# Performance work log

Hardware: AMD Instinct MI355X
Metric: run time of the kernel (lower is better)

## Reference

```python
import jax, jax.numpy as jnp
import numpy as np

B, T, C = 8, 2048, 768
N_LAYER, LAYER_ID = 12, 0


def setup_inputs() -> dict:
    key = jax.random.key(0)
    ks = jax.random.split(key, 5)
    s = 1.0 / np.sqrt(C)
    x = jax.random.normal(ks[0], (B, T, C), jnp.float32)
    Wk = jax.random.normal(ks[1], (C, C), jnp.float32) * s
    Wv = jax.random.normal(ks[2], (C, C), jnp.float32) * s
    Wr = jax.random.normal(ks[3], (C, C), jnp.float32) * s
    Wo = jax.random.normal(ks[4], (C, C), jnp.float32) * s
    # 'fancy' init for decay / first (layer_id=0 -> ratio_0_to_1 = 0)
    h = np.arange(C, dtype=np.float64)
    decay = (-5.0 + 8.0 * (h / (C - 1)) ** 0.7).astype(np.float32)
    zigzag = (((np.arange(C) + 1) % 3) - 1).astype(np.float64) * 0.5
    first = (np.log(0.3) + zigzag).astype(np.float32)
    return dict(x=x, Wk=Wk, Wv=Wv, Wr=Wr, Wo=Wo,
                decay=jnp.asarray(decay), first=jnp.asarray(first))


def _bi_wkv(w, u, k, v):
    """Bidirectional WKV (Vision-RWKV style), numerically stabilized scans.

    y_t = (sum_{i<t} e^{-(t-1-i)w + k_i} v_i + sum_{i>t} e^{-(i-1-t)w + k_i} v_i
           + e^{u + k_t} v_t) / (same with v_i -> 1).
    k, v: [B,T,C]; w, u: [C].
    """
    kT = jnp.swapaxes(k, 0, 1)  # [T,B,C]
    vT = jnp.swapaxes(v, 0, 1)
    Bb, Cc = kT.shape[1], kT.shape[2]
    NEG = jnp.float32(-1e38)

    def step(carry, inp):
        a, b, p = carry  # a = sum e^{x_i-p} v_i, b = sum e^{x_i-p}, p = running max
        kt, vt = inp
        out = (a, b, p)  # state covers strictly-earlier positions
        p_new = jnp.maximum(p - w, kt)
        e1 = jnp.exp(p - w - p_new)
        e2 = jnp.exp(kt - p_new)
        return (e1 * a + e2 * vt, e1 * b + e2, p_new), out

    init = (jnp.zeros((Bb, Cc), jnp.float32),
            jnp.zeros((Bb, Cc), jnp.float32),
            jnp.full((Bb, Cc), NEG, jnp.float32))
    _, (aL, bL, pL) = jax.lax.scan(step, init, (kT, vT))
    _, (aR, bR, pR) = jax.lax.scan(step, init, (kT[::-1], vT[::-1]))
    aR, bR, pR = aR[::-1], bR[::-1], pR[::-1]

    ps = u + kT  # self term exponent
    q = jnp.maximum(jnp.maximum(pL, pR), ps)
    eL = jnp.exp(pL - q)
    eR = jnp.exp(pR - q)
    eS = jnp.exp(ps - q)
    y = (eL * aL + eR * aR + eS * vT) / (eL * bL + eR * bR + eS)
    return jnp.swapaxes(y, 0, 1)  # [B,T,C]


def reference(x, Wk, Wv, Wr, Wo, decay, first):
    Tlen = x.shape[1]
    # shift_pixel=0 -> xk = xv = xr = x
    k = jnp.einsum('btc,oc->bto', x, Wk)
    v = jnp.einsum('btc,oc->bto', x, Wv)
    sr = jax.nn.sigmoid(jnp.einsum('btc,oc->bto', x, Wr))
    y = _bi_wkv(decay / Tlen, first / Tlen, k, v)
    return jnp.einsum('btj,cj->btc', sr * y, Wo)
```

## Files before the change

kernel.cpp:

```cpp
#include <hip/hip_runtime.h>

#define BSZ 8
#define TLEN 2048
#define CDIM 768
#define LCH 16
#define NCH (TLEN / LCH)

typedef __attribute__((ext_vector_type(4))) float f32x4;
typedef __attribute__((ext_vector_type(8))) _Float16 f16x8;
typedef __attribute__((ext_vector_type(4))) _Float16 f16x4;
typedef __attribute__((ext_vector_type(4))) float float4v;

#define GLD16(g, l)                                                          \
    __builtin_amdgcn_global_load_lds(                                        \
        (const __attribute__((address_space(1))) unsigned int*)(g),          \
        (__attribute__((address_space(3))) unsigned int*)(l), 16, 0, 0)

__global__ __launch_bounds__(256) void split_f16(const float* __restrict__ src,
                                                 _Float16* __restrict__ dst, int n4) {
    int i = blockIdx.x * 256 + threadIdx.x;
    if (i >= n4) return;
    float4v f = ((const float4v*)src)[i];
    f16x4 h;
    #pragma unroll
    for (int j = 0; j < 4; ++j) h[j] = (_Float16)f[j];
    ((f16x4*)dst)[i] = h;
}

__global__ __launch_bounds__(256, 2) void gemm_128(
    const _Float16* __restrict__ A, const _Float16* __restrict__ W,
    _Float16* __restrict__ o0, _Float16* __restrict__ o1, _Float16* __restrict__ o2,
    float* __restrict__ of32, int mpx, int NTL) {
    constexpr int K = CDIM;
    constexpr int NT = K / 64;
    __shared__ __align__(16) char smem[65536];

    const int tid  = threadIdx.x;
    const int lane = tid & 63;
    const int wid  = tid >> 6;
    const int bid  = blockIdx.x;
    const int xcd  = bid & 7;
    const int lj   = bid >> 3;
    const int mt   = lj / NTL;
    const int nt   = lj - mt * NTL;
    const int m0   = (xcd * mpx + mt) * 128;
    const int n0   = nt * 128;

    const int gq = (tid & 7) ^ ((tid >> 3) & 7);
    const char* gA = (const char*)A;
    const char* gW = (const char*)W;
    const size_t gofsA = (size_t)(m0 + (tid >> 3)) * (K * 2) + gq * 16;
    const size_t gofsB = (size_t)(n0 + (tid >> 3)) * (K * 2) + gq * 16;
    const int lofs = tid * 16;

    auto STAGE = [&](int bufb, int t) {
        const size_t kb = (size_t)t * 128;
        #pragma unroll
        for (int q = 0; q < 4; ++q) {
            GLD16(gA + gofsA + kb + (size_t)q * 49152, &smem[bufb] + lofs + q * 4096);
            GLD16(gW + gofsB + kb + (size_t)q * 49152, &smem[bufb + 16384] + lofs + q * 4096);
        }
    };

    const int wr = wid >> 1, wc = wid & 1;
    const int rl = lane & 15;
    const int kc0 = ((((lane >> 4)    ) ^ (rl & 7)) << 4);
    const int kc1 = ((((lane >> 4) + 4) ^ (rl & 7)) << 4);

    f32x4 acc[4][4];
    #pragma unroll
    for (int i = 0; i < 4; ++i)
        #pragma unroll
        for (int j = 0; j < 4; ++j)
            acc[i][j] = (f32x4){0.f, 0.f, 0.f, 0.f};

    auto COMPUTE = [&](int bufb) {
        const char* sa = &smem[bufb];
        const char* sbb = &smem[bufb + 16384];
        #pragma unroll
        for (int ks = 0; ks < 2; ++ks) {
            const int kc = ks ? kc1 : kc0;
            f16x8 a[4], b[4];
            #pragma unroll
            for (int fi = 0; fi < 4; ++fi)
                a[fi] = *(const f16x8*)(sa + (wr * 64 + fi * 16 + rl) * 128 + kc);
            #pragma unroll
            for (int fj = 0; fj < 4; ++fj)
                b[fj] = *(const f16x8*)(sbb + (wc * 64 + fj * 16 + rl) * 128 + kc);
            #pragma unroll
            for (int fi = 0; fi < 4; ++fi)
                #pragma unroll
                for (int fj = 0; fj < 4; ++fj)
                    acc[fi][fj] = __builtin_amdgcn_mfma_f32_16x16x32_f16(
                        a[fi], b[fj], acc[fi][fj], 0, 0, 0);
        }
    };

    STAGE(0, 0);
    __syncthreads();
    int buf = 0;
    for (int t = 0; t < NT; ++t) {
        if (t + 1 < NT) STAGE(buf ^ 32768, t + 1);
        COMPUTE(buf);
        __syncthreads();
        buf ^= 32768;
    }

    const int erow0 = m0 + wr * 64 + ((lane >> 4) << 2);
    if (of32) {
        const int col0 = n0 + wc * 64 + rl;
        #pragma unroll
        for (int mf = 0; mf < 4; ++mf)
            #pragma unroll
            for (int nf = 0; nf < 4; ++nf)
                #pragma unroll
                for (int r = 0; r < 4; ++r)
                    of32[(size_t)(erow0 + mf * 16 + r) * CDIM + (col0 + nf * 16)] =
                        acc[mf][nf][r];
    } else {
        const int mat  = nt / 6;
        const int col0 = (nt - mat * 6) * 128 + wc * 64 + rl;
        _Float16* o = (mat == 0) ? o0 : ((mat == 1) ? o1 : o2);
        if (mat == 2) {
            #pragma unroll
            for (int mf = 0; mf < 4; ++mf)
                #pragma unroll
                for (int nf = 0; nf < 4; ++nf)
                    #pragma unroll
                    for (int r = 0; r < 4; ++r)
                        o[(size_t)(erow0 + mf * 16 + r) * CDIM + (col0 + nf * 16)] =
                            (_Float16)(1.0f / (1.0f + __expf(-acc[mf][nf][r])));
        } else {
            #pragma unroll
            for (int mf = 0; mf < 4; ++mf)
                #pragma unroll
                for (int nf = 0; nf < 4; ++nf)
                    #pragma unroll
                    for (int r = 0; r < 4; ++r)
                        o[(size_t)(erow0 + mf * 16 + r) * CDIM + (col0 + nf * 16)] =
                            (_Float16)acc[mf][nf][r];
        }
    }
}

#define WKV_STEP(a, bb, p, kt, vt, w)                \
    {                                                \
        const float pn = fmaxf((p) - (w), (kt));     \
        const float e1 = __expf((p) - (w) - pn);     \
        const float e2 = __expf((kt) - pn);          \
        (a)  = e1 * (a)  + e2 * (vt);                \
        (bb) = e1 * (bb) + e2;                       \
        (p)  = pn;                                   \
    }

__global__ __launch_bounds__(256) void wkv_phase1(
    const _Float16* __restrict__ k, const _Float16* __restrict__ v,
    const float* __restrict__ decay,
    float* __restrict__ Sfa, float* __restrict__ Sfb, float* __restrict__ Sfp,
    float* __restrict__ Sba, float* __restrict__ Sbb, float* __restrict__ Sbp) {
    const int c = blockIdx.x * 256 + threadIdx.x;
    const int j = blockIdx.y;
    const int b = blockIdx.z;
    const float w = decay[c] * (1.0f / (float)TLEN);

    const size_t base = ((size_t)b * TLEN + (size_t)j * LCH) * CDIM + c;
    float kt[LCH], vt[LCH];
    #pragma unroll
    for (int i = 0; i < LCH; ++i) {
        kt[i] = (float)k[base + (size_t)i * CDIM];
        vt[i] = (float)v[base + (size_t)i * CDIM];
    }

    const size_t idx = ((size_t)b * NCH + j) * CDIM + c;

    float a = 0.0f, bb = 0.0f, p = -1e38f;
    #pragma unroll
    for (int i = 0; i < LCH; ++i) WKV_STEP(a, bb, p, kt[i], vt[i], w);
    Sfa[idx] = a; Sfb[idx] = bb; Sfp[idx] = p;

    a = 0.0f; bb = 0.0f; p = -1e38f;
    #pragma unroll
    for (int i = LCH - 1; i >= 0; --i) WKV_STEP(a, bb, p, kt[i], vt[i], w);
    Sba[idx] = a; Sbb[idx] = bb; Sbp[idx] = p;
}

#define WKV_COMBINE(a, bb, p, as, bs, ps, wL)        \
    {                                                \
        const float pn = fmaxf((p) - (wL), (ps));    \
        const float e1 = __expf((p) - (wL) - pn);    \
        const float e2 = __expf((ps) - pn);          \
        (a)  = e1 * (a)  + e2 * (as);                \
        (bb) = e1 * (bb) + e2 * (bs);                \
        (p)  = pn;                                   \
    }

__global__ __launch_bounds__(64) void wkv_phase2(
    const float* __restrict__ Sfa, const float* __restrict__ Sfb, const float* __restrict__ Sfp,
    const float* __restrict__ Sba, const float* __restrict__ Sbb, const float* __restrict__ Sbp,
    const float* __restrict__ decay,
    float* __restrict__ Lina, float* __restrict__ Linb, float* __restrict__ Linp,
    float* __restrict__ Rina, float* __restrict__ Rinb, float* __restrict__ Rinp) {
    const int c = blockIdx.x * 64 + threadIdx.x;
    const int b = blockIdx.y;
    const int dir = blockIdx.z;
    const float wL = decay[c] * ((float)LCH / (float)TLEN);

    const float* Sa = dir ? Sba : Sfa;
    const float* Sb = dir ? Sbb : Sfb;
    const float* Sp = dir ? Sbp : Sfp;
    float* Oa = dir ? Rina : Lina;
    float* Ob = dir ? Rinb : Linb;
    float* Op = dir ? Rinp : Linp;

    const size_t base = (size_t)b * NCH * CDIM + c;
    auto IDX = [&](int j) {
        return base + (size_t)(dir ? (NCH - 1 - j) : j) * CDIM;
    };

    float gaA[4], gbA[4], gpA[4], gaB[4], gbB[4], gpB[4];
    #pragma unroll
    for (int u = 0; u < 4; ++u) {
        const size_t id = IDX(u);
        gaA[u] = Sa[id]; gbA[u] = Sb[id]; gpA[u] = Sp[id];
    }
    float a = 0.0f, bb = 0.0f, p = -1e38f;

    for (int jg = 0; jg < NCH; jg += 8) {
        #pragma unroll
        for (int u = 0; u < 4; ++u) {
            const size_t id = IDX(jg + 4 + u);
            gaB[u] = Sa[id]; gbB[u] = Sb[id]; gpB[u] = Sp[id];
        }
        #pragma unroll
        for (int u = 0; u < 4; ++u) {
            const size_t id = IDX(jg + u);
            Oa[id] = a; Ob[id] = bb; Op[id] = p;
            WKV_COMBINE(a, bb, p, gaA[u], gbA[u], gpA[u], wL);
        }
        if (jg + 8 < NCH) {
            #pragma unroll
            for (int u = 0; u < 4; ++u) {
                const size_t id = IDX(jg + 8 + u);
                gaA[u] = Sa[id]; gbA[u] = Sb[id]; gpA[u] = Sp[id];
            }
        }
        #pragma unroll
        for (int u = 0; u < 4; ++u) {
            const size_t id = IDX(jg + 4 + u);
            Oa[id] = a; Ob[id] = bb; Op[id] = p;
            WKV_COMBINE(a, bb, p, gaB[u], gbB[u], gpB[u], wL);
        }
    }
}

__global__ __launch_bounds__(256) void wkv_phase3(
    const _Float16* __restrict__ k, const _Float16* __restrict__ v,
    const _Float16* __restrict__ sr,
    const float* __restrict__ Lina, const float* __restrict__ Linb, const float* __restrict__ Linp,
    const float* __restrict__ Rina, const float* __restrict__ Rinb, const float* __restrict__ Rinp,
    const float* __restrict__ decay, const float* __restrict__ first,
    _Float16* __restrict__ zh) {
    const int c = blockIdx.x * 256 + threadIdx.x;
    const int j = blockIdx.y;
    const int b = blockIdx.z;
    const float w = decay[c] * (1.0f / (float)TLEN);
    const float u = first[c] * (1.0f / (float)TLEN);

    const size_t base = ((size_t)b * TLEN + (size_t)j * LCH) * CDIM + c;
    float kt[LCH], vt[LCH];
    #pragma unroll
    for (int i = 0; i < LCH; ++i) {
        kt[i] = (float)k[base + (size_t)i * CDIM];
        vt[i] = (float)v[base + (size_t)i * CDIM];
    }

    const size_t idx = ((size_t)b * NCH + j) * CDIM + c;

    float ar[LCH], br[LCH], pr[LCH];
    {
        float a = Rina[idx], bb = Rinb[idx], p = Rinp[idx];
        #pragma unroll
        for (int i = LCH - 1; i >= 0; --i) {
            ar[i] = a; br[i] = bb; pr[i] = p;
            WKV_STEP(a, bb, p, kt[i], vt[i], w);
        }
    }
    {
        float a = Lina[idx], bb = Linb[idx], p = Linp[idx];
        #pragma unroll
        for (int i = 0; i < LCH; ++i) {
            const size_t off = base + (size_t)i * CDIM;
            const float srt = (float)sr[off];
            const float ps = u + kt[i];
            const float q  = fmaxf(fmaxf(p, pr[i]), ps);
            const float eL = __expf(p - q);
            const float eR = __expf(pr[i] - q);
            const float eS = __expf(ps - q);
            const float num = eL * a  + eR * ar[i] + eS * vt[i];
            const float den = eL * bb + eR * br[i] + eS;
            zh[off] = (_Float16)(srt * (num / den));
            WKV_STEP(a, bb, p, kt[i], vt[i], w);
        }
    }
}

extern "C" void kernel_launch(void* const* d_in, const int* in_sizes, int n_in,
                              void* d_out, int out_size, void* d_ws, size_t ws_size,
                              hipStream_t stream) {
    const float* x     = (const float*)d_in[0];
    const float* Wk    = (const float*)d_in[1];
    const float* Wv    = (const float*)d_in[2];
    const float* Wr    = (const float*)d_in[3];
    const float* Wo    = (const float*)d_in[4];
    const float* decay = (const float*)d_in[5];
    const float* first = (const float*)d_in[6];
    float* out = (float*)d_out;

    const size_t WN = (size_t)CDIM * CDIM;
    const size_t wbytes = 4 * WN * sizeof(_Float16);
    const size_t per_b  = (size_t)TLEN * CDIM * 8 + 12ull * NCH * CDIM * 4;
    if (ws_size < wbytes + per_b) return;
    int nb = (int)((ws_size - wbytes) / per_b);
    if (nb > BSZ) nb = BSZ;

    _Float16* wsp  = (_Float16*)d_ws;
    _Float16* Wcat = wsp;
    _Float16* Woh  = wsp + 3 * WN;

    const size_t NE = (size_t)nb * TLEN * CDIM;
    const size_t NP = (size_t)nb * NCH * CDIM;
    float* Sfa = (float*)(wsp + 4 * WN);
    float* Sfb = Sfa + NP;  float* Sfp = Sfb + NP;
    float* Sba = Sfp + NP;  float* Sbb = Sba + NP;  float* Sbp = Sbb + NP;
    float* Lina = Sbp + NP; float* Linb = Lina + NP; float* Linp = Linb + NP;
    float* Rina = Linp + NP; float* Rinb = Rina + NP; float* Rinp = Rinb + NP;
    _Float16* kh  = (_Float16*)(Rinp + NP);
    _Float16* vh  = kh + NE;
    _Float16* srh = vh + NE;
    _Float16* xh  = srh + NE;
    _Float16* zh  = xh;

    split_f16<<<dim3((int)(WN / 1024)), dim3(256), 0, stream>>>(Wk, Wcat + 0 * WN, (int)(WN / 4));
    split_f16<<<dim3((int)(WN / 1024)), dim3(256), 0, stream>>>(Wv, Wcat + 1 * WN, (int)(WN / 4));
    split_f16<<<dim3((int)(WN / 1024)), dim3(256), 0, stream>>>(Wr, Wcat + 2 * WN, (int)(WN / 4));
    split_f16<<<dim3((int)(WN / 1024)), dim3(256), 0, stream>>>(Wo, Woh, (int)(WN / 4));

    for (int b0 = 0; b0 < BSZ; b0 += nb) {
        const int curb = (BSZ - b0 < nb) ? (BSZ - b0) : nb;
        const int rows = curb * TLEN;
        const float* xc = x   + (size_t)b0 * TLEN * CDIM;
        float*       oc = out + (size_t)b0 * TLEN * CDIM;

        const int n4 = rows * CDIM / 4;
        split_f16<<<dim3(n4 / 256), dim3(256), 0, stream>>>(xc, xh, n4);

        const int mtiles = rows / 128;
        const int mpx    = mtiles / 8;

        gemm_128<<<dim3(mtiles * 18), dim3(256), 0, stream>>>(
            xh, Wcat, kh, vh, srh, nullptr, mpx, 18);

        wkv_phase1<<<dim3(CDIM / 256, NCH, curb), dim3(256), 0, stream>>>(
            kh, vh, decay, Sfa, Sfb, Sfp, Sba, Sbb, Sbp);
        wkv_phase2<<<dim3(CDIM / 64, curb, 2), dim3(64), 0, stream>>>(
            Sfa, Sfb, Sfp, Sba, Sbb, Sbp, decay,
            Lina, Linb, Linp, Rina, Rinb, Rinp);
        wkv_phase3<<<dim3(CDIM / 256, NCH, curb), dim3(256), 0, stream>>>(
            kh, vh, srh, Lina, Linb, Linp, Rina, Rinb, Rinp, decay, first, zh);

        gemm_128<<<dim3(mtiles * 6), dim3(256), 0, stream>>>(
            zh, Woh, nullptr, nullptr, nullptr, oc, mpx, 6);
    }
}
```

Measured before the change: 169.6 us.

## Vectorize WKV phases to two channels per thread and merge weight conversions

Measured after the change: 178.8 us. 1.05x slower.

```diff
diff --git a/kernel.cpp b/kernel.cpp
--- a/kernel.cpp
+++ b/kernel.cpp
@@ -10,6 +10,24 @@
 typedef __attribute__((ext_vector_type(8))) _Float16 f16x8;
 typedef __attribute__((ext_vector_type(4))) _Float16 f16x4;
 typedef __attribute__((ext_vector_type(4))) float float4v;
+typedef __attribute__((ext_vector_type(2))) float float2v;
+
+__device__ __forceinline__ float lo16(unsigned u) {
+    unsigned short s = (unsigned short)u;
+    _Float16 h; __builtin_memcpy(&h, &s, 2);
+    return (float)h;
+}
+__device__ __forceinline__ float hi16(unsigned u) {
+    unsigned short s = (unsigned short)(u >> 16);
+    _Float16 h; __builtin_memcpy(&h, &s, 2);
+    return (float)h;
+}
+__device__ __forceinline__ unsigned packf16(float x, float y) {
+    _Float16 hx = (_Float16)x, hy = (_Float16)y;
+    unsigned short sx, sy;
+    __builtin_memcpy(&sx, &hx, 2); __builtin_memcpy(&sy, &hy, 2);
+    return (unsigned)sx | ((unsigned)sy << 16);
+}
 
 #define GLD16(g, l)                                                          \
     __builtin_amdgcn_global_load_lds(                                        \
@@ -20,6 +38,22 @@
                                                  _Float16* __restrict__ dst, int n4) {
     int i = blockIdx.x * 256 + threadIdx.x;
     if (i >= n4) return;
+    float4v f = ((const float4v*)src)[i];
+    f16x4 h;
+    #pragma unroll
+    for (int j = 0; j < 4; ++j) h[j] = (_Float16)f[j];
+    ((f16x4*)dst)[i] = h;
+}
+
+__global__ __launch_bounds__(256) void split_w4(
+    const float* __restrict__ Wk, const float* __restrict__ Wv,
+    const float* __restrict__ Wr, const float* __restrict__ Wo,
+    _Float16* __restrict__ Wcat, _Float16* __restrict__ Woh, int n4) {
+    int i = blockIdx.x * 256 + threadIdx.x;
+    if (i >= n4) return;
+    const int plane = blockIdx.y;
+    const float* src = (plane == 0) ? Wk : (plane == 1) ? Wv : (plane == 2) ? Wr : Wo;
+    _Float16* dst = (plane < 3) ? (Wcat + (size_t)plane * CDIM * CDIM) : Woh;
     float4v f = ((const float4v*)src)[i];
     f16x4 h;
     #pragma unroll
@@ -41,8 +75,8 @@
     const int bid  = blockIdx.x;
     const int xcd  = bid & 7;
     const int lj   = bid >> 3;
-    const int mt   = lj / NTL;
-    const int nt   = lj - mt * NTL;
+    const int nt   = lj / mpx;
+    const int mt   = lj - nt * mpx;
     const int m0   = (xcd * mpx + mt) * 128;
     const int n0   = nt * 128;
 
@@ -153,35 +187,50 @@
         (p)  = pn;                                   \
     }
 
-__global__ __launch_bounds__(256) void wkv_phase1(
+__global__ __launch_bounds__(384) void wkv_phase1(
     const _Float16* __restrict__ k, const _Float16* __restrict__ v,
     const float* __restrict__ decay,
     float* __restrict__ Sfa, float* __restrict__ Sfb, float* __restrict__ Sfp,
     float* __restrict__ Sba, float* __restrict__ Sbb, float* __restrict__ Sbp) {
-    const int c = blockIdx.x * 256 + threadIdx.x;
-    const int j = blockIdx.y;
-    const int b = blockIdx.z;
-    const float w = decay[c] * (1.0f / (float)TLEN);
-
-    const size_t base = ((size_t)b * TLEN + (size_t)j * LCH) * CDIM + c;
-    float kt[LCH], vt[LCH];
+    const int c0 = threadIdx.x * 2;
+    const int j = blockIdx.x;
+    const int b = blockIdx.y;
+    const float2v d2 = *(const float2v*)(decay + c0);
+    const float w0 = d2.x * (1.0f / (float)TLEN);
+    const float w1 = d2.y * (1.0f / (float)TLEN);
+
+    const size_t base = ((size_t)b * TLEN + (size_t)j * LCH) * CDIM + c0;
+    unsigned kt2[LCH], vt2[LCH];
     #pragma unroll
     for (int i = 0; i < LCH; ++i) {
-        kt[i] = (float)k[base + (size_t)i * CDIM];
-        vt[i] = (float)v[base + (size_t)i * CDIM];
-    }
-
-    const size_t idx = ((size_t)b * NCH + j) * CDIM + c;
-
-    float a = 0.0f, bb = 0.0f, p = -1e38f;
-    #pragma unroll
-    for (int i = 0; i < LCH; ++i) WKV_STEP(a, bb, p, kt[i], vt[i], w);
-    Sfa[idx] = a; Sfb[idx] = bb; Sfp[idx] = p;
-
-    a = 0.0f; bb = 0.0f; p = -1e38f;
-    #pragma unroll
-    for (int i = LCH - 1; i >= 0; --i) WKV_STEP(a, bb, p, kt[i], vt[i], w);
-    Sba[idx] = a; Sbb[idx] = bb; Sbp[idx] = p;
+        kt2[i] = *(const unsigned*)(k + base + (size_t)i * CDIM);
+        vt2[i] = *(const unsigned*)(v + base + (size_t)i * CDIM);
+    }
+
+    const size_t idx = ((size_t)b * NCH + j) * CDIM + c0;
+
+    {
+        float a0 = 0.f, b0 = 0.f, p0 = -1e38f, a1 = 0.f, b1 = 0.f, p1 = -1e38f;
+        #pragma unroll
+        for (int i = 0; i < LCH; ++i) {
+            WKV_STEP(a0, b0, p0, lo16(kt2[i]), lo16(vt2[i]), w0);
+            WKV_STEP(a1, b1, p1, hi16(kt2[i]), hi16(vt2[i]), w1);
+        }
+        *(float2v*)(Sfa + idx) = (float2v){a0, a1};
+        *(float2v*)(Sfb + idx) = (float2v){b0, b1};
+        *(float2v*)(Sfp + idx) = (float2v){p0, p1};
+    }
+    {
+        float a0 = 0.f, b0 = 0.f, p0 = -1e38f, a1 = 0.f, b1 = 0.f, p1 = -1e38f;
+        #pragma unroll
+        for (int i = LCH - 1; i >= 0; --i) {
+            WKV_STEP(a0, b0, p0, lo16(kt2[i]), lo16(vt2[i]), w0);
+            WKV_STEP(a1, b1, p1, hi16(kt2[i]), hi16(vt2[i]), w1);
+        }
+        *(float2v*)(Sba + idx) = (float2v){a0, a1};
+        *(float2v*)(Sbb + idx) = (float2v){b0, b1};
+        *(float2v*)(Sbp + idx) = (float2v){p0, p1};
+    }
 }
 
 #define WKV_COMBINE(a, bb, p, as, bs, ps, wL)        \
@@ -200,10 +249,12 @@
     const float* __restrict__ decay,
     float* __restrict__ Lina, float* __restrict__ Linb, float* __restrict__ Linp,
     float* __restrict__ Rina, float* __restrict__ Rinb, float* __restrict__ Rinp) {
-    const int c = blockIdx.x * 64 + threadIdx.x;
+    const int c0 = (blockIdx.x * 64 + threadIdx.x) * 2;
     const int b = blockIdx.y;
     const int dir = blockIdx.z;
-    const float wL = decay[c] * ((float)LCH / (float)TLEN);
+    const float2v d2 = *(const float2v*)(decay + c0);
+    const float wL0 = d2.x * ((float)LCH / (float)TLEN);
+    const float wL1 = d2.y * ((float)LCH / (float)TLEN);
 
     const float* Sa = dir ? Sba : Sfa;
     const float* Sb = dir ? Sbb : Sfb;
@@ -212,94 +263,136 @@
     float* Ob = dir ? Rinb : Linb;
     float* Op = dir ? Rinp : Linp;
 
-    const size_t base = (size_t)b * NCH * CDIM + c;
+    const size_t base = (size_t)b * NCH * CDIM + c0;
     auto IDX = [&](int j) {
         return base + (size_t)(dir ? (NCH - 1 - j) : j) * CDIM;
     };
 
-    float gaA[4], gbA[4], gpA[4], gaB[4], gbB[4], gpB[4];
+    float2v gaA[4], gbA[4], gpA[4], gaB[4], gbB[4], gpB[4];
     #pragma unroll
     for (int u = 0; u < 4; ++u) {
         const size_t id = IDX(u);
-        gaA[u] = Sa[id]; gbA[u] = Sb[id]; gpA[u] = Sp[id];
-    }
-    float a = 0.0f, bb = 0.0f, p = -1e38f;
+        gaA[u] = *(const float2v*)(Sa + id);
+        gbA[u] = *(const float2v*)(Sb + id);
+        gpA[u] = *(const float2v*)(Sp + id);
+    }
+    float a0 = 0.f, b0 = 0.f, p0 = -1e38f, a1 = 0.f, b1 = 0.f, p1 = -1e38f;
 
     for (int jg = 0; jg < NCH; jg += 8) {
         #pragma unroll
         for (int u = 0; u < 4; ++u) {
             const size_t id = IDX(jg + 4 + u);
-            gaB[u] = Sa[id]; gbB[u] = Sb[id]; gpB[u] = Sp[id];
+            gaB[u] = *(const float2v*)(Sa + id);
+            gbB[u] = *(const float2v*)(Sb + id);
+            gpB[u] = *(const float2v*)(Sp + id);
         }
         #pragma unroll
         for (int u = 0; u < 4; ++u) {
             const size_t id = IDX(jg + u);
-            Oa[id] = a; Ob[id] = bb; Op[id] = p;
-            WKV_COMBINE(a, bb, p, gaA[u], gbA[u], gpA[u], wL);
+            *(float2v*)(Oa + id) = (float2v){a0, a1};
+            *(float2v*)(Ob + id) = (float2v){b0, b1};
+            *(float2v*)(Op + id) = (float2v){p0, p1};
+            WKV_COMBINE(a0, b0, p0, gaA[u].x, gbA[u].x, gpA[u].x, wL0);
+            WKV_COMBINE(a1, b1, p1, gaA[u].y, gbA[u].y, gpA[u].y, wL1);
         }
         if (jg + 8 < NCH) {
             #pragma unroll
             for (int u = 0; u < 4; ++u) {
                 const size_t id = IDX(jg + 8 + u);
-                gaA[u] = Sa[id]; gbA[u] = Sb[id]; gpA[u] = Sp[id];
+                gaA[u] = *(const float2v*)(Sa + id);
+                gbA[u] = *(const float2v*)(Sb + id);
+                gpA[u] = *(const float2v*)(Sp + id);
             }
         }
         #pragma unroll
         for (int u = 0; u < 4; ++u) {
             const size_t id = IDX(jg + 4 + u);
-            Oa[id] = a; Ob[id] = bb; Op[id] = p;
-            WKV_COMBINE(a, bb, p, gaB[u], gbB[u], gpB[u], wL);
-        }
-    }
-}
-
-__global__ __launch_bounds__(256) void wkv_phase3(
+            *(float2v*)(Oa + id) = (float2v){a0, a1};
+            *(float2v*)(Ob + id) = (float2v){b0, b1};
+            *(float2v*)(Op + id) = (float2v){p0, p1};
+            WKV_COMBINE(a0, b0, p0, gaB[u].x, gbB[u].x, gpB[u].x, wL0);
+            WKV_COMBINE(a1, b1, p1, gaB[u].y, gbB[u].y, gpB[u].y, wL1);
+        }
+    }
+}
+
+__global__ __launch_bounds__(384) void wkv_phase3(
     const _Float16* __restrict__ k, const _Float16* __restrict__ v,
     const _Float16* __restrict__ sr,
     const float* __restrict__ Lina, const float* __restrict__ Linb, const float* __restrict__ Linp,
     const float* __restrict__ Rina, const float* __restrict__ Rinb, const float* __restrict__ Rinp,
     const float* __restrict__ decay, const float* __restrict__ first,
     _Float16* __restrict__ zh) {
-    const int c = blockIdx.x * 256 + threadIdx.x;
-    const int j = blockIdx.y;
-    const int b = blockIdx.z;
-    const float w = decay[c] * (1.0f / (float)TLEN);
-    const float u = first[c] * (1.0f / (float)TLEN);
-
-    const size_t base = ((size_t)b * TLEN + (size_t)j * LCH) * CDIM + c;
-    float kt[LCH], vt[LCH];
+    const int c0 = threadIdx.x * 2;
+    const int j = blockIdx.x;
+    const int b = blockIdx.y;
+    const float2v d2 = *(const float2v*)(decay + c0);
+    const float2v f2 = *(const float2v*)(first + c0);
+    const float w0 = d2.x * (1.0f / (float)TLEN);
+    const float w1 = d2.y * (1.0f / (float)TLEN);
+    const float u0 = f2.x * (1.0f / (float)TLEN);
+    const float u1 = f2.y * (1.0f / (float)TLEN);
+
+    const size_t base = ((size_t)b * TLEN + (size_t)j * LCH) * CDIM + c0;
+    unsigned kt2[LCH], vt2[LCH];
     #pragma unroll
     for (int i = 0; i < LCH; ++i) {
-        kt[i] = (float)k[base + (size_t)i * CDIM];
-        vt[i] = (float)v[base + (size_t)i * CDIM];
-    }
-
-    const size_t idx = ((size_t)b * NCH + j) * CDIM + c;
-
-    float ar[LCH], br[LCH], pr[LCH];
+        kt2[i] = *(const unsigned*)(k + base + (size_t)i * CDIM);
+        vt2[i] = *(const unsigned*)(v + base + (size_t)i * CDIM);
+    }
+
+    const size_t idx = ((size_t)b * NCH + j) * CDIM + c0;
+
+    float ar0[LCH], br0[LCH], pr0[LCH], ar1[LCH], br1[LCH], pr1[LCH];
     {
-        float a = Rina[idx], bb = Rinb[idx], p = Rinp[idx];
+        float2v ra = *(const float2v*)(Rina + idx);
+        float2v rb = *(const float2v*)(Rinb + idx);
+        float2v rp = *(const float2v*)(Rinp + idx);
+        float a0 = ra.x, b0 = rb.x, p0 = rp.x;
+        float a1 = ra.y, b1 = rb.y, p1 = rp.y;
         #pragma unroll
         for (int i = LCH - 1; i >= 0; --i) {
-            ar[i] = a; br[i] = bb; pr[i] = p;
-            WKV_STEP(a, bb, p, kt[i], vt[i], w);
+            ar0[i] = a0; br0[i] = b0; pr0[i] = p0;
+            ar1[i] = a1; br1[i] = b1; pr1[i] = p1;
+            WKV_STEP(a0, b0, p0, lo16(kt2[i]), lo16(vt2[i]), w0);
+            WKV_STEP(a1, b1, p1, hi16(kt2[i]), hi16(vt2[i]), w1);
         }
     }
     {
-        float a = Lina[idx], bb = Linb[idx], p = Linp[idx];
+        float2v la = *(const float2v*)(Lina + idx);
+        float2v lb = *(const float2v*)(Linb + idx);
+        float2v lp = *(const float2v*)(Linp + idx);
+        float a0 = la.x, b0 = lb.x, p0 = lp.x;
+        float a1 = la.y, b1 = lb.y, p1 = lp.y;
         #pragma unroll
         for (int i = 0; i < LCH; ++i) {
             const size_t off = base + (size_t)i * CDIM;
-            const float srt = (float)sr[off];
-            const float ps = u + kt[i];
-            const float q  = fmaxf(fmaxf(p, pr[i]), ps);
-            const float eL = __expf(p - q);
-            const float eR = __expf(pr[i] - q);
-            const float eS = __expf(ps - q);
-            const float num = eL * a  + eR * ar[i] + eS * vt[i];
-            const float den = eL * bb + eR * br[i] + eS;
-            zh[off] = (_Float16)(srt * (num / den));
-            WKV_STEP(a, bb, p, kt[i], vt[i], w);
+            const unsigned sr2 = *(const unsigned*)(sr + off);
+            const float kk0 = lo16(kt2[i]), vv0 = lo16(vt2[i]);
+            const float kk1 = hi16(kt2[i]), vv1 = hi16(vt2[i]);
+
+            const float ps0 = u0 + kk0;
+            const float q0  = fmaxf(fmaxf(p0, pr0[i]), ps0);
+            const float eL0 = __expf(p0 - q0);
+            const float eR0 = __expf(pr0[i] - q0);
+            const float eS0 = __expf(ps0 - q0);
+            const float y0 = (eL0 * a0 + eR0 * ar0[i] + eS0 * vv0) /
+                             (eL0 * b0 + eR0 * br0[i] + eS0);
+            const float z0 = lo16(sr2) * y0;
+
+            const float ps1 = u1 + kk1;
+            const float q1  = fmaxf(fmaxf(p1, pr1[i]), ps1);
+            const float eL1 = __expf(p1 - q1);
+            const float eR1 = __expf(pr1[i] - q1);
+            const float eS1 = __expf(ps1 - q1);
+            const float y1 = (eL1 * a1 + eR1 * ar1[i] + eS1 * vv1) /
+                             (eL1 * b1 + eR1 * br1[i] + eS1);
+            const float z1 = hi16(sr2) * y1;
+
+            *(unsigned*)(zh + off) = packf16(z0, z1);
+
+            WKV_STEP(a0, b0, p0, kk0, vv0, w0);
+            WKV_STEP(a1, b1, p1, kk1, vv1, w1);
         }
     }
 }
@@ -340,10 +433,8 @@
     _Float16* xh  = srh + NE;
     _Float16* zh  = xh;
 
-    split_f16<<<dim3((int)(WN / 1024)), dim3(256), 0, stream>>>(Wk, Wcat + 0 * WN, (int)(WN / 4));
-    split_f16<<<dim3((int)(WN / 1024)), dim3(256), 0, stream>>>(Wv, Wcat + 1 * WN, (int)(WN / 4));
-    split_f16<<<dim3((int)(WN / 1024)), dim3(256), 0, stream>>>(Wr, Wcat + 2 * WN, (int)(WN / 4));
-    split_f16<<<dim3((int)(WN / 1024)), dim3(256), 0, stream>>>(Wo, Woh, (int)(WN / 4));
+    split_w4<<<dim3((int)(WN / 1024), 4), dim3(256), 0, stream>>>(
+        Wk, Wv, Wr, Wo, Wcat, Woh, (int)(WN / 4));
 
     for (int b0 = 0; b0 < BSZ; b0 += nb) {
         const int curb = (BSZ - b0 < nb) ? (BSZ - b0) : nb;
@@ -360,12 +451,12 @@
         gemm_128<<<dim3(mtiles * 18), dim3(256), 0, stream>>>(
             xh, Wcat, kh, vh, srh, nullptr, mpx, 18);
 
-        wkv_phase1<<<dim3(CDIM / 256, NCH, curb), dim3(256), 0, stream>>>(
+        wkv_phase1<<<dim3(NCH, curb), dim3(384), 0, stream>>>(
             kh, vh, decay, Sfa, Sfb, Sfp, Sba, Sbb, Sbp);
-        wkv_phase2<<<dim3(CDIM / 64, curb, 2), dim3(64), 0, stream>>>(
+        wkv_phase2<<<dim3(CDIM / 128, curb, 2), dim3(64), 0, stream>>>(
             Sfa, Sfb, Sfp, Sba, Sbb, Sbp, decay,
             Lina, Linb, Linp, Rina, Rinb, Rinp);
-        wkv_phase3<<<dim3(CDIM / 256, NCH, curb), dim3(256), 0, stream>>>(
+        wkv_phase3<<<dim3(NCH, curb), dim3(384), 0, stream>>>(
             kh, vh, srh, Lina, Linb, Linp, Rina, Rinb, Rinp, decay, first, zh);
 
         gemm_128<<<dim3(mtiles * 6), dim3(256), 0, stream>>>(
```

## Fuse weight conversions, reorder GEMM tile mapping, vectorize WKV phase1 channel pairs

Applied to the files above, without the earlier changes.

Result: faster. 163.2 us (-3.8%).

```diff
diff --git a/kernel.cpp b/kernel.cpp
--- a/kernel.cpp
+++ b/kernel.cpp
@@ -10,6 +10,18 @@
 typedef __attribute__((ext_vector_type(8))) _Float16 f16x8;
 typedef __attribute__((ext_vector_type(4))) _Float16 f16x4;
 typedef __attribute__((ext_vector_type(4))) float float4v;
+typedef __attribute__((ext_vector_type(2))) float float2v;
+
+__device__ __forceinline__ float lo16(unsigned u) {
+    unsigned short s = (unsigned short)u;
+    _Float16 h; __builtin_memcpy(&h, &s, 2);
+    return (float)h;
+}
+__device__ __forceinline__ float hi16(unsigned u) {
+    unsigned short s = (unsigned short)(u >> 16);
+    _Float16 h; __builtin_memcpy(&h, &s, 2);
+    return (float)h;
+}
 
 #define GLD16(g, l)                                                          \
     __builtin_amdgcn_global_load_lds(                                        \
@@ -20,6 +32,22 @@
                                                  _Float16* __restrict__ dst, int n4) {
     int i = blockIdx.x * 256 + threadIdx.x;
     if (i >= n4) return;
+    float4v f = ((const float4v*)src)[i];
+    f16x4 h;
+    #pragma unroll
+    for (int j = 0; j < 4; ++j) h[j] = (_Float16)f[j];
+    ((f16x4*)dst)[i] = h;
+}
+
+__global__ __launch_bounds__(256) void split_w4(
+    const float* __restrict__ Wk, const float* __restrict__ Wv,
+    const float* __restrict__ Wr, const float* __restrict__ Wo,
+    _Float16* __restrict__ Wcat, _Float16* __restrict__ Woh, int n4) {
+    int i = blockIdx.x * 256 + threadIdx.x;
+    if (i >= n4) return;
+    const int plane = blockIdx.y;
+    const float* src = (plane == 0) ? Wk : (plane == 1) ? Wv : (plane == 2) ? Wr : Wo;
+    _Float16* dst = (plane < 3) ? (Wcat + (size_t)plane * CDIM * CDIM) : Woh;
     float4v f = ((const float4v*)src)[i];
     f16x4 h;
     #pragma unroll
@@ -41,8 +69,8 @@
     const int bid  = blockIdx.x;
     const int xcd  = bid & 7;
     const int lj   = bid >> 3;
-    const int mt   = lj / NTL;
-    const int nt   = lj - mt * NTL;
+    const int nt   = lj / mpx;
+    const int mt   = lj - nt * mpx;
     const int m0   = (xcd * mpx + mt) * 128;
     const int n0   = nt * 128;
 
@@ -153,35 +181,50 @@
         (p)  = pn;                                   \
     }
 
-__global__ __launch_bounds__(256) void wkv_phase1(
+__global__ __launch_bounds__(384) void wkv_phase1(
     const _Float16* __restrict__ k, const _Float16* __restrict__ v,
     const float* __restrict__ decay,
     float* __restrict__ Sfa, float* __restrict__ Sfb, float* __restrict__ Sfp,
     float* __restrict__ Sba, float* __restrict__ Sbb, float* __restrict__ Sbp) {
-    const int c = blockIdx.x * 256 + threadIdx.x;
-    const int j = blockIdx.y;
-    const int b = blockIdx.z;
-    const float w = decay[c] * (1.0f / (float)TLEN);
-
-    const size_t base = ((size_t)b * TLEN + (size_t)j * LCH) * CDIM + c;
-    float kt[LCH], vt[LCH];
+    const int c0 = threadIdx.x * 2;
+    const int j = blockIdx.x;
+    const int b = blockIdx.y;
+    const float2v d2 = *(const float2v*)(decay + c0);
+    const float w0 = d2.x * (1.0f / (float)TLEN);
+    const float w1 = d2.y * (1.0f / (float)TLEN);
+
+    const size_t base = ((size_t)b * TLEN + (size_t)j * LCH) * CDIM + c0;
+    unsigned kt2[LCH], vt2[LCH];
     #pragma unroll
     for (int i = 0; i < LCH; ++i) {
-        kt[i] = (float)k[base + (size_t)i * CDIM];
-        vt[i] = (float)v[base + (size_t)i * CDIM];
-    }
-
-    const size_t idx = ((size_t)b * NCH + j) * CDIM + c;
-
-    float a = 0.0f, bb = 0.0f, p = -1e38f;
-    #pragma unroll
-    for (int i = 0; i < LCH; ++i) WKV_STEP(a, bb, p, kt[i], vt[i], w);
-    Sfa[idx] = a; Sfb[idx] = bb; Sfp[idx] = p;
-
-    a = 0.0f; bb = 0.0f; p = -1e38f;
-    #pragma unroll
-    for (int i = LCH - 1; i >= 0; --i) WKV_STEP(a, bb, p, kt[i], vt[i], w);
-    Sba[idx] = a; Sbb[idx] = bb; Sbp[idx] = p;
+        kt2[i] = *(const unsigned*)(k + base + (size_t)i * CDIM);
+        vt2[i] = *(const unsigned*)(v + base + (size_t)i * CDIM);
+    }
+
+    const size_t idx = ((size_t)b * NCH + j) * CDIM + c0;
+
+    {
+        float a0 = 0.f, b0 = 0.f, p0 = -1e38f, a1 = 0.f, b1 = 0.f, p1 = -1e38f;
+        #pragma unroll
+        for (int i = 0; i < LCH; ++i) {
+            WKV_STEP(a0, b0, p0, lo16(kt2[i]), lo16(vt2[i]), w0);
+            WKV_STEP(a1, b1, p1, hi16(kt2[i]), hi16(vt2[i]), w1);
+        }
+        *(float2v*)(Sfa + idx) = (float2v){a0, a1};
+        *(float2v*)(Sfb + idx) = (float2v){b0, b1};
+        *(float2v*)(Sfp + idx) = (float2v){p0, p1};
+    }
+    {
+        float a0 = 0.f, b0 = 0.f, p0 = -1e38f, a1 = 0.f, b1 = 0.f, p1 = -1e38f;
+        #pragma unroll
+        for (int i = LCH - 1; i >= 0; --i) {
+            WKV_STEP(a0, b0, p0, lo16(kt2[i]), lo16(vt2[i]), w0);
+            WKV_STEP(a1, b1, p1, hi16(kt2[i]), hi16(vt2[i]), w1);
+        }
+        *(float2v*)(Sba + idx) = (float2v){a0, a1};
+        *(float2v*)(Sbb + idx) = (float2v){b0, b1};
+        *(float2v*)(Sbp + idx) = (float2v){p0, p1};
+    }
 }
 
 #define WKV_COMBINE(a, bb, p, as, bs, ps, wL)        \
@@ -340,10 +383,8 @@
     _Float16* xh  = srh + NE;
     _Float16* zh  = xh;
 
-    split_f16<<<dim3((int)(WN / 1024)), dim3(256), 0, stream>>>(Wk, Wcat + 0 * WN, (int)(WN / 4));
-    split_f16<<<dim3((int)(WN / 1024)), dim3(256), 0, stream>>>(Wv, Wcat + 1 * WN, (int)(WN / 4));
-    split_f16<<<dim3((int)(WN / 1024)), dim3(256), 0, stream>>>(Wr, Wcat + 2 * WN, (int)(WN / 4));
-    split_f16<<<dim3((int)(WN / 1024)), dim3(256), 0, stream>>>(Wo, Woh, (int)(WN / 4));
+    split_w4<<<dim3((int)(WN / 1024), 4), dim3(256), 0, stream>>>(
+        Wk, Wv, Wr, Wo, Wcat, Woh, (int)(WN / 4));
 
     for (int b0 = 0; b0 < BSZ; b0 += nb) {
         const int curb = (BSZ - b0 < nb) ? (BSZ - b0) : nb;
@@ -360,7 +401,7 @@
         gemm_128<<<dim3(mtiles * 18), dim3(256), 0, stream>>>(
             xh, Wcat, kh, vh, srh, nullptr, mpx, 18);
 
-        wkv_phase1<<<dim3(CDIM / 256, NCH, curb), dim3(256), 0, stream>>>(
+        wkv_phase1<<<dim3(NCH, curb), dim3(384), 0, stream>>>(
             kh, vh, decay, Sfa, Sfb, Sfp, Sba, Sbb, Sbp);
         wkv_phase2<<<dim3(CDIM / 64, curb, 2), dim3(64), 0, stream>>>(
             Sfa, Sfb, Sfp, Sba, Sbb, Sbp, decay,
```
